# Performance work log

Hardware: AMD Instinct MI355X
Metric: run time of the kernel (lower is better)

## Reference

```python
import jax, jax.numpy as jnp
import numpy as np

N_QUBITS = 10
N_LAYERS = 2
BATCH = 8192
N_PARAMS = 5 * N_QUBITS * N_LAYERS  # 100
C64 = jnp.complex64

# ---- batched 2x2 gate matrices (theta: (B,)) ----

def _rx(theta):
    h = theta * 0.5
    c = jnp.cos(h).astype(C64)
    s = (-1j * jnp.sin(h).astype(C64))
    return jnp.stack([jnp.stack([c, s], -1), jnp.stack([s, c], -1)], -2)

def _ry(theta):
    h = theta * 0.5
    c = jnp.cos(h).astype(C64)
    s = jnp.sin(h).astype(C64)
    return jnp.stack([jnp.stack([c, -s], -1), jnp.stack([s, c], -1)], -2)

def _rz(theta):
    h = theta.astype(jnp.float32) * 0.5
    e0 = jnp.exp(-1j * h.astype(C64))
    e1 = jnp.exp(1j * h.astype(C64))
    z = jnp.zeros_like(e0)
    return jnp.stack([jnp.stack([e0, z], -1), jnp.stack([z, e1], -1)], -2)

# psi layout: (B, 2, 2, ..., 2); axis 1+w corresponds to wire w (PennyLane order: wire 0 = MSB)

def _apply_1q(psi, mat, w):
    psi = jnp.moveaxis(psi, 1 + w, -1)
    sh = psi.shape
    out = jnp.einsum('bij,bkj->bki', mat, psi.reshape(sh[0], -1, 2))
    return jnp.moveaxis(out.reshape(sh), -1, 1 + w)

def _apply_crx(psi, theta, ctrl, tgt):
    psi = jnp.moveaxis(psi, [1 + ctrl, 1 + tgt], [-2, -1])
    sh = psi.shape
    p = psi.reshape(sh[0], -1, 2, 2)  # axes: (batch, rest, ctrl, tgt)
    h = theta * 0.5
    c = jnp.cos(h)[:, None].astype(C64)
    s = (-1j * jnp.sin(h)[:, None].astype(C64))
    a0 = p[..., 1, 0]
    a1 = p[..., 1, 1]
    p1 = jnp.stack([c * a0 + s * a1, s * a0 + c * a1], -1)
    p = jnp.stack([p[..., 0, :], p1], -2)
    return jnp.moveaxis(p.reshape(sh), [-2, -1], [1 + ctrl, 1 + tgt])

def _init_state(angles):
    B = angles.shape[0]
    psi = jnp.zeros((B, 2 ** N_QUBITS), C64).at[:, 0].set(1.0)
    psi = psi.reshape((B,) + (2,) * N_QUBITS)
    for i in range(N_QUBITS):  # RY input embedding
        psi = _apply_1q(psi, _ry(angles[:, i]), i)
    return psi

def _delta_layer(psi, params, dt, off):
    for i in range(N_QUBITS):
        psi = _apply_1q(psi, _rx(params[:, off] * dt), i)
        psi = _apply_1q(psi, _ry(params[:, off + 1] * dt), i)
        psi = _apply_1q(psi, _rz(params[:, off + 2] * dt), i)
        off += 3
    for i in range(N_QUBITS):
        psi = _apply_crx(psi, params[:, off], i, (i + 1) % N_QUBITS); off += 1
    for i in range(N_QUBITS - 1, -1, -1):
        psi = _apply_crx(psi, params[:, off], i, (i - 1) % N_QUBITS); off += 1
    return psi, off

def _backward_layer(psi, params, dt, off):
    for i in range(N_QUBITS - 1, -1, -1):
        psi = _apply_1q(psi, _rx(params[:, off] * dt), i)
        psi = _apply_1q(psi, _ry(params[:, off + 1] * dt), i)
        psi = _apply_1q(psi, _rz(params[:, off + 2] * dt), i)
        off += 3
    for i in range(N_QUBITS - 1, -1, -1):
        psi = _apply_crx(psi, params[:, off], i, (i - 1) % N_QUBITS); off += 1
    for i in range(N_QUBITS):
        psi = _apply_crx(psi, params[:, off], i, (i + 1) % N_QUBITS); off += 1
    return psi, off

def _unified_layer(psi, params, off):
    for i in range(N_QUBITS):
        psi = _apply_1q(psi, _rx(params[:, off]), i)
        psi = _apply_1q(psi, _ry(params[:, off + 1]), i)
        psi = _apply_1q(psi, _rz(params[:, off + 2]), i)
        off += 3
    for i in range(N_QUBITS):
        psi = _apply_crx(psi, params[:, off], i, (i + 1) % N_QUBITS); off += 1
    for i in range(N_QUBITS - 1, -1, -1):
        psi = _apply_crx(psi, params[:, off], i, (i - 1) % N_QUBITS); off += 1
    return psi, off

def _forward_circuit(angles, params, dt):
    psi = _init_state(angles); off = 0
    for _ in range(N_LAYERS):
        psi, off = _delta_layer(psi, params, dt, off)
    return psi.reshape(psi.shape[0], -1)

def _backward_circuit(angles, params, dt):
    psi = _init_state(angles); off = 0
    for _ in range(N_LAYERS):
        psi, off = _backward_layer(psi, params, dt, off)
    return psi.reshape(psi.shape[0], -1)

def _diagonal_circuit(angles, params):
    psi = _init_state(angles); off = 0
    for _ in range(N_LAYERS):
        psi, off = _unified_layer(psi, params, off)
    return psi.reshape(psi.shape[0], -1)

def _measure(psi_flat):
    # Pauli X/Y/Z expectations per qubit -> (B, 3*n_qubits), ordered [X..., Y..., Z...]
    B = psi_flat.shape[0]
    t = psi_flat.reshape((B,) + (2,) * N_QUBITS)
    Xs, Ys, Zs = [], [], []
    for w in range(N_QUBITS):
        p = jnp.moveaxis(t, 1 + w, -1).reshape(B, -1, 2)
        cross = jnp.sum(jnp.conj(p[..., 0]) * p[..., 1], axis=1)
        Xs.append(2.0 * cross.real)
        Ys.append(2.0 * cross.imag)
        Zs.append(jnp.sum(jnp.abs(p[..., 0]) ** 2 - jnp.abs(p[..., 1]) ** 2, axis=1))
    return jnp.stack(Xs + Ys + Zs, axis=1)

def setup_inputs() -> dict:
    key = jax.random.key(0)
    k1, k2, k3, k4, k5 = jax.random.split(key, 5)
    init_val = np.float32(1.0 / np.sqrt(3.0))
    return {
        'input_angles': jax.random.normal(k1, (BATCH, N_QUBITS), jnp.float32),
        'forward_params': jax.random.normal(k2, (BATCH, N_PARAMS), jnp.float32),
        'backward_params': jax.random.normal(k3, (BATCH, N_PARAMS), jnp.float32),
        'diagonal_params': jax.random.normal(k4, (BATCH, N_PARAMS), jnp.float32),
        'dt_scale': jax.random.uniform(k5, (BATCH,), jnp.float32),
        'alpha_real': jnp.asarray(init_val), 'alpha_imag': jnp.asarray(0.0, jnp.float32),
        'beta_real': jnp.asarray(init_val), 'beta_imag': jnp.asarray(0.0, jnp.float32),
        'gamma_real': jnp.asarray(init_val), 'gamma_imag': jnp.asarray(0.0, jnp.float32),
    }

def reference(input_angles, forward_params, backward_params, diagonal_params, dt_scale,
              alpha_real, alpha_imag, beta_real, beta_imag, gamma_real, gamma_imag):
    psi1 = _forward_circuit(input_angles, forward_params, dt_scale)
    psi2 = _backward_circuit(input_angles, backward_params, dt_scale)
    psi3 = _diagonal_circuit(input_angles, diagonal_params)
    alpha = jax.lax.complex(alpha_real, alpha_imag).astype(C64)
    beta = jax.lax.complex(beta_real, beta_imag).astype(C64)
    gamma = jax.lax.complex(gamma_real, gamma_imag).astype(C64)
    norm = jnp.sqrt(jnp.abs(alpha) ** 2 + jnp.abs(beta) ** 2 + jnp.abs(gamma) ** 2 + 1e-9).astype(C64)
    psi = (alpha / norm) * psi1 + (beta / norm) * psi2 + (gamma / norm) * psi3
    vnorm = jnp.linalg.norm(psi, axis=-1, keepdims=True) + 1e-9
    psi = psi / vnorm.astype(C64)
    return _measure(psi).astype(jnp.float32)
```

## Files before the change

kernel.cpp:

```cpp
#include <hip/hip_runtime.h>

#define NQ    10
#define NPRM  100
#define NBATCH 8192

using F2 = float2;

template<int LM>
__device__ __forceinline__ float lshf(float v) {
  if constexpr (LM == 1) {
    int r = __builtin_amdgcn_update_dpp(0, __builtin_bit_cast(int, v), 0xB1, 0xF, 0xF, true);
    return __builtin_bit_cast(float, r);
  } else if constexpr (LM == 2) {
    int r = __builtin_amdgcn_update_dpp(0, __builtin_bit_cast(int, v), 0x4E, 0xF, 0xF, true);
    return __builtin_bit_cast(float, r);
  } else if constexpr (LM == 8) {
    int r = __builtin_amdgcn_update_dpp(0, __builtin_bit_cast(int, v), 0x128, 0xF, 0xF, true);
    return __builtin_bit_cast(float, r);
  } else {
    return __shfl_xor(v, LM, 64);
  }
}



template<int P>
__device__ __forceinline__ void g_rx(F2* st, unsigned lane, float c, float s) {
  if constexpr (P < 4) {
    constexpr int m = 1 << P;
#pragma unroll
    for (int r = 0; r < 16; ++r) if (!(r & m)) {
      const int r1 = r | m;
      F2 a0 = st[r], a1 = st[r1];
      st[r]  = F2{c*a0.x + s*a1.y, c*a0.y - s*a1.x};
      st[r1] = F2{s*a0.y + c*a1.x, c*a1.y - s*a0.x};
    }
  } else {
    constexpr int lm = 1 << (P - 4);
#pragma unroll
    for (int r = 0; r < 16; ++r) {
      float mx = st[r].x, my = st[r].y;
      float ox = lshf<lm>(mx), oy = lshf<lm>(my);
      st[r] = F2{c*mx + s*oy, c*my - s*ox};
    }
  }
}


template<int P>
__device__ __forceinline__ void g_u(F2* st, unsigned lane, F2 u00, F2 u01) {
  if constexpr (P < 4) {
    constexpr int m = 1 << P;
#pragma unroll
    for (int r = 0; r < 16; ++r) if (!(r & m)) {
      const int r1 = r | m;
      F2 a0 = st[r], a1 = st[r1];
      st[r]  = F2{u00.x*a0.x - u00.y*a0.y + u01.x*a1.x - u01.y*a1.y,
                  u00.x*a0.y + u00.y*a0.x + u01.x*a1.y + u01.y*a1.x};
      st[r1] = F2{-u01.x*a0.x - u01.y*a0.y + u00.x*a1.x + u00.y*a1.y,
                  -u01.x*a0.y + u01.y*a0.x + u00.x*a1.y - u00.y*a1.x};
    }
  } else {
    constexpr int lm = 1 << (P - 4);
    const bool hi = (lane & lm) != 0;
    const float vax = u00.x,               vay = hi ? -u00.y : u00.y;
    const float vbx = hi ? -u01.x : u01.x, vby = u01.y;
#pragma unroll
    for (int r = 0; r < 16; ++r) {
      float mx = st[r].x, my = st[r].y;
      float ox = lshf<lm>(mx), oy = lshf<lm>(my);
      st[r] = F2{vax*mx - vay*my + vbx*ox - vby*oy,
                 vax*my + vay*mx + vbx*oy + vby*ox};
    }
  }
}


template<int TB, int CB>
__device__ __forceinline__ void g_crx(F2* st, unsigned lane, float c, float s) {
  if constexpr (CB >= 4) {
    const bool act = (lane >> (CB - 4)) & 1u;
    const float ce = act ? c : 1.0f;
    const float se = act ? s : 0.0f;
    g_rx<TB>(st, lane, ce, se);
  } else {
    constexpr int cm = 1 << CB;
    if constexpr (TB < 4) {
#pragma unroll
      for (int r = 0; r < 16; ++r) if ((r & cm) && !(r & (1 << TB))) {
        const int r1 = r | (1 << TB);
        F2 a0 = st[r], a1 = st[r1];
        st[r]  = F2{c*a0.x + s*a1.y, c*a0.y - s*a1.x};
        st[r1] = F2{s*a0.y + c*a1.x, c*a1.y - s*a0.x};
      }
    } else {
      constexpr int lm = 1 << (TB - 4);
#pragma unroll
      for (int r = 0; r < 16; ++r) if (r & cm) {
        float mx = st[r].x, my = st[r].y;
        float ox = lshf<lm>(mx), oy = lshf<lm>(my);
        st[r] = F2{c*mx + s*oy, c*my - s*ox};
      }
    }
  }
}


__device__ __forceinline__ void g_u_w(F2* st, unsigned lane, int w, F2 u00, F2 u01) {
  switch (w) {
    case 0: g_u<9>(st,lane,u00,u01); break;
    case 1: g_u<8>(st,lane,u00,u01); break;
    case 2: g_u<7>(st,lane,u00,u01); break;
    case 3: g_u<6>(st,lane,u00,u01); break;
    case 4: g_u<5>(st,lane,u00,u01); break;
    case 5: g_u<4>(st,lane,u00,u01); break;
    case 6: g_u<3>(st,lane,u00,u01); break;
    case 7: g_u<2>(st,lane,u00,u01); break;
    case 8: g_u<1>(st,lane,u00,u01); break;
    case 9: g_u<0>(st,lane,u00,u01); break;
  }
}

#define CRX_CASE(CW,TW) case (CW)*10+(TW): g_crx<9-(TW), 9-(CW)>(st,lane,c,s); break;
__device__ __forceinline__ void crx_w(F2* st, unsigned lane, int cw, int tw, float c, float s) {
  switch (cw * 10 + tw) {
    CRX_CASE(0,1) CRX_CASE(1,2) CRX_CASE(2,3) CRX_CASE(3,4) CRX_CASE(4,5)
    CRX_CASE(5,6) CRX_CASE(6,7) CRX_CASE(7,8) CRX_CASE(8,9) CRX_CASE(9,0)
    CRX_CASE(1,0) CRX_CASE(2,1) CRX_CASE(3,2) CRX_CASE(4,3) CRX_CASE(5,4)
    CRX_CASE(6,5) CRX_CASE(7,6) CRX_CASE(8,7) CRX_CASE(9,8) CRX_CASE(0,9)
  }
}

__device__ __forceinline__ void make_u(float ax, float ay, float az, F2& u00, F2& u01) {
  float ca, sa, cb, sb, cg, sg;
  __sincosf(ax*0.5f, &sa, &ca);
  __sincosf(ay*0.5f, &sb, &cb);
  __sincosf(az*0.5f, &sg, &cg);
  const float m00x =  cb*ca, m00y =  sb*sa;
  const float m01x = -sb*ca, m01y = -cb*sa;
  u00 = F2{m00x*cg + m00y*sg, m00y*cg - m00x*sg};
  u01 = F2{m01x*cg + m01y*sg, m01y*cg - m01x*sg};
}


__device__ __forceinline__ void layer_fwd(F2* st, unsigned lane, const float* P, float dt, int& off) {
#pragma unroll
  for (int i = 0; i < NQ; ++i) {
    F2 u00, u01;
    make_u(P[off]*dt, P[off+1]*dt, P[off+2]*dt, u00, u01);
    g_u_w(st, lane, i, u00, u01);
    off += 3;
  }
#pragma unroll
  for (int i = 0; i < NQ; ++i) {
    float s, c; __sincosf(P[off]*0.5f, &s, &c);
    crx_w(st, lane, i, (i+1)%NQ, c, s); ++off;
  }
#pragma unroll
  for (int i = NQ-1; i >= 0; --i) {
    float s, c; __sincosf(P[off]*0.5f, &s, &c);
    crx_w(st, lane, i, (i+NQ-1)%NQ, c, s); ++off;
  }
}

__device__ __forceinline__ void layer_bwd(F2* st, unsigned lane, const float* P, float dt, int& off) {
#pragma unroll
  for (int i = NQ-1; i >= 0; --i) {
    F2 u00, u01;
    make_u(P[off]*dt, P[off+1]*dt, P[off+2]*dt, u00, u01);
    g_u_w(st, lane, i, u00, u01);
    off += 3;
  }
#pragma unroll
  for (int i = NQ-1; i >= 0; --i) {
    float s, c; __sincosf(P[off]*0.5f, &s, &c);
    crx_w(st, lane, i, (i+NQ-1)%NQ, c, s); ++off;
  }
#pragma unroll
  for (int i = 0; i < NQ; ++i) {
    float s, c; __sincosf(P[off]*0.5f, &s, &c);
    crx_w(st, lane, i, (i+1)%NQ, c, s); ++off;
  }
}

__device__ __forceinline__ void init_state(F2* st, unsigned lane, const float* ang) {
  float cw[NQ], sw[NQ];
#pragma unroll
  for (int w = 0; w < NQ; ++w) __sincosf(ang[w]*0.5f, &sw[w], &cw[w]);
  float L = 1.0f;
#pragma unroll
  for (int q = 0; q < 6; ++q)
    L *= ((lane >> q) & 1u) ? sw[5-q] : cw[5-q];
#pragma unroll
  for (int r = 0; r < 16; ++r) {
    float R = L;
#pragma unroll
    for (int p = 0; p < 4; ++p)
      R *= ((r >> p) & 1) ? sw[9-p] : cw[9-p];
    st[r] = F2{R, 0.0f};
  }
}


template<int P>
__device__ __forceinline__ void meas(const F2* st, unsigned lane, float& X, float& Y, float& Z) {
  float cr = 0.f, ci = 0.f, z = 0.f;
  if constexpr (P < 4) {
    constexpr int m = 1 << P;
#pragma unroll
    for (int r = 0; r < 16; ++r) if (!(r & m)) {
      const int r1 = r | m;
      F2 a0 = st[r], a1 = st[r1];
      cr += a0.x*a1.x + a0.y*a1.y;
      ci += a0.x*a1.y - a0.y*a1.x;
      z  += (a0.x*a0.x + a0.y*a0.y) - (a1.x*a1.x + a1.y*a1.y);
    }
    cr *= 2.f; ci *= 2.f;
  } else {
    constexpr int lm = 1 << (P - 4);
    const bool hi = (lane & lm) != 0;
#pragma unroll
    for (int r = 0; r < 16; ++r) {
      float mx = st[r].x, my = st[r].y;
      float ox = lshf<lm>(mx), oy = lshf<lm>(my);
      float a0x = hi ? ox : mx, a0y = hi ? oy : my;
      float a1x = hi ? mx : ox, a1y = hi ? my : oy;
      cr += a0x*a1x + a0y*a1y;
      ci += a0x*a1y - a0y*a1x;
      float p2 = mx*mx + my*my;
      z += hi ? -p2 : p2;
    }
  }
  X = cr; Y = ci; Z = z;
}

__device__ __forceinline__ float wred(float v) {
  v += lshf<1>(v);
  v += lshf<2>(v);
  v += lshf<4>(v);
  v += lshf<8>(v);
  v += lshf<16>(v);
  v += lshf<32>(v);
  return v;
}


__global__ void __launch_bounds__(256) qsim_kernel(
    const float* __restrict__ angles, const float* __restrict__ fwdP,
    const float* __restrict__ bwdP,   const float* __restrict__ diagP,
    const float* __restrict__ dts,
    const float* __restrict__ ar, const float* __restrict__ ai,
    const float* __restrict__ br, const float* __restrict__ bi,
    const float* __restrict__ gr, const float* __restrict__ gi,
    float* __restrict__ out)
{
  const int tid = blockIdx.x * blockDim.x + threadIdx.x;
  const int b = tid >> 6;
  if (b >= NBATCH) return;
  const unsigned lane = threadIdx.x & 63u;
  const int bu = __builtin_amdgcn_readfirstlane(b);

  const float* ang = angles + bu * NQ;
  const float dt = dts[bu];

  const float arv = ar[0], aiv = ai[0], brv = br[0], biv = bi[0], grv = gr[0], giv = gi[0];
  const float nrm = sqrtf(arv*arv + aiv*aiv + brv*brv + biv*biv + grv*grv + giv*giv + 1e-9f);
  const F2 cA{arv/nrm, aiv/nrm}, cB{brv/nrm, biv/nrm}, cG{grv/nrm, giv/nrm};

  F2 st[16], acc[16];

  init_state(st, lane, ang);
  { int off = 0; const float* P = fwdP + bu*NPRM;
#pragma unroll
    for (int l = 0; l < 2; ++l) layer_fwd(st, lane, P, dt, off); }
#pragma unroll
  for (int r = 0; r < 16; ++r)
    acc[r] = F2{cA.x*st[r].x - cA.y*st[r].y, cA.x*st[r].y + cA.y*st[r].x};

  init_state(st, lane, ang);
  { int off = 0; const float* P = bwdP + bu*NPRM;
#pragma unroll
    for (int l = 0; l < 2; ++l) layer_bwd(st, lane, P, dt, off); }
#pragma unroll
  for (int r = 0; r < 16; ++r) {
    acc[r].x += cB.x*st[r].x - cB.y*st[r].y;
    acc[r].y += cB.x*st[r].y + cB.y*st[r].x;
  }

  init_state(st, lane, ang);
  { int off = 0; const float* P = diagP + bu*NPRM;
#pragma unroll
    for (int l = 0; l < 2; ++l) layer_fwd(st, lane, P, 1.0f, off); }
#pragma unroll
  for (int r = 0; r < 16; ++r) {
    acc[r].x += cG.x*st[r].x - cG.y*st[r].y;
    acc[r].y += cG.x*st[r].y + cG.y*st[r].x;
  }

  float n2 = 0.f;
#pragma unroll
  for (int r = 0; r < 16; ++r) n2 += acc[r].x*acc[r].x + acc[r].y*acc[r].y;
  n2 = wred(n2);
  const float inv = 1.0f / (sqrtf(n2) + 1e-9f);
#pragma unroll
  for (int r = 0; r < 16; ++r) { acc[r].x *= inv; acc[r].y *= inv; }

  float* o = out + b * 30;
#pragma unroll
  for (int w = 0; w < NQ; ++w) {
    float X, Y, Z;
    switch (w) {
      case 0: meas<9>(acc, lane, X, Y, Z); break;
      case 1: meas<8>(acc, lane, X, Y, Z); break;
      case 2: meas<7>(acc, lane, X, Y, Z); break;
      case 3: meas<6>(acc, lane, X, Y, Z); break;
      case 4: meas<5>(acc, lane, X, Y, Z); break;
      case 5: meas<4>(acc, lane, X, Y, Z); break;
      case 6: meas<3>(acc, lane, X, Y, Z); break;
      case 7: meas<2>(acc, lane, X, Y, Z); break;
      case 8: meas<1>(acc, lane, X, Y, Z); break;
      default: meas<0>(acc, lane, X, Y, Z); break;
    }
    X = wred(X); Y = wred(Y); Z = wred(Z);
    if (lane == 0) { o[w] = X; o[10 + w] = Y; o[20 + w] = Z; }
  }
}

extern "C" void kernel_launch(void* const* d_in, const int* in_sizes, int n_in,
                              void* d_out, int out_size, void* d_ws, size_t ws_size,
                              hipStream_t stream) {
  const float* angles = (const float*)d_in[0];
  const float* fwdP   = (const float*)d_in[1];
  const float* bwdP   = (const float*)d_in[2];
  const float* diagP  = (const float*)d_in[3];
  const float* dts    = (const float*)d_in[4];
  const float* ar     = (const float*)d_in[5];
  const float* ai     = (const float*)d_in[6];
  const float* br     = (const float*)d_in[7];
  const float* bi     = (const float*)d_in[8];
  const float* gr     = (const float*)d_in[9];
  const float* gi     = (const float*)d_in[10];
  float* out = (float*)d_out;

  const int threads = 256;
  const int blocks  = NBATCH / (threads / 64);
  qsim_kernel<<<blocks, threads, 0, stream>>>(
      angles, fwdP, bwdP, diagP, dts, ar, ai, br, bi, gr, gi, out);
}
```

Before: 257.3 us.

## Simulate forward and diagonal circuits together in packed float2 SoA lanes

The forward and diagonal circuits share the same gate structure, so both are now simulated in one pass. Each amplitude is stored as separate real and imaginary float2 vectors, where the x component holds the forward circuit and the y component holds the diagonal one, so the compiler can emit packed FP32 math (v_pk_fma_f32). This removes one full serial circuit simulation and turns the per-element complex math into packed operations. In exchange it doubles the live state registers during that pass, which risks register pressure and lower occupancy, and it still shuffles each half of the vector separately.

```diff
diff --git a/kernel.cpp b/kernel.cpp
--- a/kernel.cpp
+++ b/kernel.cpp
@@ -4,7 +4,10 @@
 #define NPRM  100
 #define NBATCH 8192
 
-using F2 = float2;
+using F2 = __attribute__((ext_vector_type(2))) float;
+
+__device__ __forceinline__ F2 mk2(float a, float b) { F2 v; v.x = a; v.y = b; return v; }
+
 
 template<int LM>
 __device__ __forceinline__ float lshf(float v) {
@@ -21,6 +24,10 @@
     return __shfl_xor(v, LM, 64);
   }
 }
+template<int LM>
+__device__ __forceinline__ F2 lshf2(F2 v) {
+  return mk2(lshf<LM>(v.x), lshf<LM>(v.y));
+}
 
 
 
@@ -32,8 +39,8 @@
     for (int r = 0; r < 16; ++r) if (!(r & m)) {
       const int r1 = r | m;
       F2 a0 = st[r], a1 = st[r1];
-      st[r]  = F2{c*a0.x + s*a1.y, c*a0.y - s*a1.x};
-      st[r1] = F2{s*a0.y + c*a1.x, c*a1.y - s*a0.x};
+      st[r]  = mk2(c*a0.x + s*a1.y, c*a0.y - s*a1.x);
+      st[r1] = mk2(s*a0.y + c*a1.x, c*a1.y - s*a0.x);
     }
   } else {
     constexpr int lm = 1 << (P - 4);
@@ -41,11 +48,10 @@
     for (int r = 0; r < 16; ++r) {
       float mx = st[r].x, my = st[r].y;
       float ox = lshf<lm>(mx), oy = lshf<lm>(my);
-      st[r] = F2{c*mx + s*oy, c*my - s*ox};
-    }
-  }
-}
-
+      st[r] = mk2(c*mx + s*oy, c*my - s*ox);
+    }
+  }
+}
 
 template<int P>
 __device__ __forceinline__ void g_u(F2* st, unsigned lane, F2 u00, F2 u01) {
@@ -55,10 +61,10 @@
     for (int r = 0; r < 16; ++r) if (!(r & m)) {
       const int r1 = r | m;
       F2 a0 = st[r], a1 = st[r1];
-      st[r]  = F2{u00.x*a0.x - u00.y*a0.y + u01.x*a1.x - u01.y*a1.y,
-                  u00.x*a0.y + u00.y*a0.x + u01.x*a1.y + u01.y*a1.x};
-      st[r1] = F2{-u01.x*a0.x - u01.y*a0.y + u00.x*a1.x + u00.y*a1.y,
-                  -u01.x*a0.y + u01.y*a0.x + u00.x*a1.y - u00.y*a1.x};
+      st[r]  = mk2(u00.x*a0.x - u00.y*a0.y + u01.x*a1.x - u01.y*a1.y,
+                   u00.x*a0.y + u00.y*a0.x + u01.x*a1.y + u01.y*a1.x);
+      st[r1] = mk2(-u01.x*a0.x - u01.y*a0.y + u00.x*a1.x + u00.y*a1.y,
+                   -u01.x*a0.y + u01.y*a0.x + u00.x*a1.y - u00.y*a1.x);
     }
   } else {
     constexpr int lm = 1 << (P - 4);
@@ -69,12 +75,11 @@
     for (int r = 0; r < 16; ++r) {
       float mx = st[r].x, my = st[r].y;
       float ox = lshf<lm>(mx), oy = lshf<lm>(my);
-      st[r] = F2{vax*mx - vay*my + vbx*ox - vby*oy,
-                 vax*my + vay*mx + vbx*oy + vby*ox};
-    }
-  }
-}
-
+      st[r] = mk2(vax*mx - vay*my + vbx*ox - vby*oy,
+                  vax*my + vay*mx + vbx*oy + vby*ox);
+    }
+  }
+}
 
 template<int TB, int CB>
 __device__ __forceinline__ void g_crx(F2* st, unsigned lane, float c, float s) {
@@ -90,8 +95,8 @@
       for (int r = 0; r < 16; ++r) if ((r & cm) && !(r & (1 << TB))) {
         const int r1 = r | (1 << TB);
         F2 a0 = st[r], a1 = st[r1];
-        st[r]  = F2{c*a0.x + s*a1.y, c*a0.y - s*a1.x};
-        st[r1] = F2{s*a0.y + c*a1.x, c*a1.y - s*a0.x};
+        st[r]  = mk2(c*a0.x + s*a1.y, c*a0.y - s*a1.x);
+        st[r1] = mk2(s*a0.y + c*a1.x, c*a1.y - s*a0.x);
       }
     } else {
       constexpr int lm = 1 << (TB - 4);
@@ -99,12 +104,11 @@
       for (int r = 0; r < 16; ++r) if (r & cm) {
         float mx = st[r].x, my = st[r].y;
         float ox = lshf<lm>(mx), oy = lshf<lm>(my);
-        st[r] = F2{c*mx + s*oy, c*my - s*ox};
+        st[r] = mk2(c*mx + s*oy, c*my - s*ox);
       }
     }
   }
 }
-
 
 __device__ __forceinline__ void g_u_w(F2* st, unsigned lane, int w, F2 u00, F2 u01) {
   switch (w) {
@@ -138,29 +142,8 @@
   __sincosf(az*0.5f, &sg, &cg);
   const float m00x =  cb*ca, m00y =  sb*sa;
   const float m01x = -sb*ca, m01y = -cb*sa;
-  u00 = F2{m00x*cg + m00y*sg, m00y*cg - m00x*sg};
-  u01 = F2{m01x*cg + m01y*sg, m01y*cg - m01x*sg};
-}
-
-
-__device__ __forceinline__ void layer_fwd(F2* st, unsigned lane, const float* P, float dt, int& off) {
-#pragma unroll
-  for (int i = 0; i < NQ; ++i) {
-    F2 u00, u01;
-    make_u(P[off]*dt, P[off+1]*dt, P[off+2]*dt, u00, u01);
-    g_u_w(st, lane, i, u00, u01);
-    off += 3;
-  }
-#pragma unroll
-  for (int i = 0; i < NQ; ++i) {
-    float s, c; __sincosf(P[off]*0.5f, &s, &c);
-    crx_w(st, lane, i, (i+1)%NQ, c, s); ++off;
-  }
-#pragma unroll
-  for (int i = NQ-1; i >= 0; --i) {
-    float s, c; __sincosf(P[off]*0.5f, &s, &c);
-    crx_w(st, lane, i, (i+NQ-1)%NQ, c, s); ++off;
-  }
+  u00 = mk2(m00x*cg + m00y*sg, m00y*cg - m00x*sg);
+  u01 = mk2(m01x*cg + m01y*sg, m01y*cg - m01x*sg);
 }
 
 __device__ __forceinline__ void layer_bwd(F2* st, unsigned lane, const float* P, float dt, int& off) {
@@ -197,7 +180,168 @@
 #pragma unroll
     for (int p = 0; p < 4; ++p)
       R *= ((r >> p) & 1) ? sw[9-p] : cw[9-p];
-    st[r] = F2{R, 0.0f};
+    st[r] = mk2(R, 0.0f);
+  }
+}
+
+
+struct UU { F2 x00, y00, x01, y01; };
+
+template<int P>
+__device__ __forceinline__ void g_u2(F2* sR, F2* sI, unsigned lane, UU u) {
+  if constexpr (P < 4) {
+    constexpr int m = 1 << P;
+#pragma unroll
+    for (int r = 0; r < 16; ++r) if (!(r & m)) {
+      const int r1 = r | m;
+      F2 R0 = sR[r], I0 = sI[r], R1 = sR[r1], I1 = sI[r1];
+      sR[r]  = u.x00*R0 - u.y00*I0 + u.x01*R1 - u.y01*I1;
+      sI[r]  = u.x00*I0 + u.y00*R0 + u.x01*I1 + u.y01*R1;
+      sR[r1] = u.x00*R1 + u.y00*I1 - u.x01*R0 - u.y01*I0;
+      sI[r1] = u.x00*I1 - u.y00*R1 - u.x01*I0 + u.y01*R0;
+    }
+  } else {
+    constexpr int lm = 1 << (P - 4);
+    const bool hi = (lane & lm) != 0;
+    const F2 vay = mk2(hi ? -u.y00.x : u.y00.x, hi ? -u.y00.y : u.y00.y);
+    const F2 vbx = mk2(hi ? -u.x01.x : u.x01.x, hi ? -u.x01.y : u.x01.y);
+#pragma unroll
+    for (int r = 0; r < 16; ++r) {
+      F2 R = sR[r], I = sI[r];
+      F2 oR = lshf2<lm>(R), oI = lshf2<lm>(I);
+      sR[r] = u.x00*R - vay*I + vbx*oR - u.y01*oI;
+      sI[r] = u.x00*I + vay*R + vbx*oI + u.y01*oR;
+    }
+  }
+}
+
+template<int P>
+__device__ __forceinline__ void g_rx2(F2* sR, F2* sI, unsigned lane, F2 C, F2 S) {
+  if constexpr (P < 4) {
+    constexpr int m = 1 << P;
+#pragma unroll
+    for (int r = 0; r < 16; ++r) if (!(r & m)) {
+      const int r1 = r | m;
+      F2 R0 = sR[r], I0 = sI[r], R1 = sR[r1], I1 = sI[r1];
+      sR[r]  = C*R0 + S*I1;
+      sI[r]  = C*I0 - S*R1;
+      sR[r1] = C*R1 + S*I0;
+      sI[r1] = C*I1 - S*R0;
+    }
+  } else {
+    constexpr int lm = 1 << (P - 4);
+#pragma unroll
+    for (int r = 0; r < 16; ++r) {
+      F2 R = sR[r], I = sI[r];
+      F2 oR = lshf2<lm>(R), oI = lshf2<lm>(I);
+      sR[r] = C*R + S*oI;
+      sI[r] = C*I - S*oR;
+    }
+  }
+}
+
+template<int TB, int CB>
+__device__ __forceinline__ void g_crx2(F2* sR, F2* sI, unsigned lane, F2 C, F2 S) {
+  if constexpr (CB >= 4) {
+    const bool act = (lane >> (CB - 4)) & 1u;
+    const F2 Ce = mk2(act ? C.x : 1.0f, act ? C.y : 1.0f);
+    const F2 Se = mk2(act ? S.x : 0.0f, act ? S.y : 0.0f);
+    g_rx2<TB>(sR, sI, lane, Ce, Se);
+  } else {
+    constexpr int cm = 1 << CB;
+    if constexpr (TB < 4) {
+#pragma unroll
+      for (int r = 0; r < 16; ++r) if ((r & cm) && !(r & (1 << TB))) {
+        const int r1 = r | (1 << TB);
+        F2 R0 = sR[r], I0 = sI[r], R1 = sR[r1], I1 = sI[r1];
+        sR[r]  = C*R0 + S*I1;
+        sI[r]  = C*I0 - S*R1;
+        sR[r1] = C*R1 + S*I0;
+        sI[r1] = C*I1 - S*R0;
+      }
+    } else {
+      constexpr int lm = 1 << (TB - 4);
+#pragma unroll
+      for (int r = 0; r < 16; ++r) if (r & cm) {
+        F2 R = sR[r], I = sI[r];
+        F2 oR = lshf2<lm>(R), oI = lshf2<lm>(I);
+        sR[r] = C*R + S*oI;
+        sI[r] = C*I - S*oR;
+      }
+    }
+  }
+}
+
+__device__ __forceinline__ void g_u2_w(F2* sR, F2* sI, unsigned lane, int w, UU u) {
+  switch (w) {
+    case 0: g_u2<9>(sR,sI,lane,u); break;
+    case 1: g_u2<8>(sR,sI,lane,u); break;
+    case 2: g_u2<7>(sR,sI,lane,u); break;
+    case 3: g_u2<6>(sR,sI,lane,u); break;
+    case 4: g_u2<5>(sR,sI,lane,u); break;
+    case 5: g_u2<4>(sR,sI,lane,u); break;
+    case 6: g_u2<3>(sR,sI,lane,u); break;
+    case 7: g_u2<2>(sR,sI,lane,u); break;
+    case 8: g_u2<1>(sR,sI,lane,u); break;
+    case 9: g_u2<0>(sR,sI,lane,u); break;
+  }
+}
+
+#define CRX2_CASE(CW,TW) case (CW)*10+(TW): g_crx2<9-(TW), 9-(CW)>(sR,sI,lane,C,S); break;
+__device__ __forceinline__ void crx2_w(F2* sR, F2* sI, unsigned lane, int cw, int tw, F2 C, F2 S) {
+  switch (cw * 10 + tw) {
+    CRX2_CASE(0,1) CRX2_CASE(1,2) CRX2_CASE(2,3) CRX2_CASE(3,4) CRX2_CASE(4,5)
+    CRX2_CASE(5,6) CRX2_CASE(6,7) CRX2_CASE(7,8) CRX2_CASE(8,9) CRX2_CASE(9,0)
+    CRX2_CASE(1,0) CRX2_CASE(2,1) CRX2_CASE(3,2) CRX2_CASE(4,3) CRX2_CASE(5,4)
+    CRX2_CASE(6,5) CRX2_CASE(7,6) CRX2_CASE(8,7) CRX2_CASE(9,8) CRX2_CASE(0,9)
+  }
+}
+
+__device__ __forceinline__ void layer_fwd2(F2* sR, F2* sI, unsigned lane,
+                                           const float* Pf, const float* Pd, float dt, int& off) {
+#pragma unroll
+  for (int i = 0; i < NQ; ++i) {
+    F2 u00F, u01F, u00D, u01D;
+    make_u(Pf[off]*dt, Pf[off+1]*dt, Pf[off+2]*dt, u00F, u01F);
+    make_u(Pd[off],    Pd[off+1],    Pd[off+2],    u00D, u01D);
+    UU u;
+    u.x00 = mk2(u00F.x, u00D.x); u.y00 = mk2(u00F.y, u00D.y);
+    u.x01 = mk2(u01F.x, u01D.x); u.y01 = mk2(u01F.y, u01D.y);
+    g_u2_w(sR, sI, lane, i, u);
+    off += 3;
+  }
+#pragma unroll
+  for (int i = 0; i < NQ; ++i) {
+    float sF, cF, sD, cD;
+    __sincosf(Pf[off]*0.5f, &sF, &cF);
+    __sincosf(Pd[off]*0.5f, &sD, &cD);
+    crx2_w(sR, sI, lane, i, (i+1)%NQ, mk2(cF,cD), mk2(sF,sD)); ++off;
+  }
+#pragma unroll
+  for (int i = NQ-1; i >= 0; --i) {
+    float sF, cF, sD, cD;
+    __sincosf(Pf[off]*0.5f, &sF, &cF);
+    __sincosf(Pd[off]*0.5f, &sD, &cD);
+    crx2_w(sR, sI, lane, i, (i+NQ-1)%NQ, mk2(cF,cD), mk2(sF,sD)); ++off;
+  }
+}
+
+__device__ __forceinline__ void init_state2(F2* sR, F2* sI, unsigned lane, const float* ang) {
+  float cw[NQ], sw[NQ];
+#pragma unroll
+  for (int w = 0; w < NQ; ++w) __sincosf(ang[w]*0.5f, &sw[w], &cw[w]);
+  float L = 1.0f;
+#pragma unroll
+  for (int q = 0; q < 6; ++q)
+    L *= ((lane >> q) & 1u) ? sw[5-q] : cw[5-q];
+#pragma unroll
+  for (int r = 0; r < 16; ++r) {
+    float R = L;
+#pragma unroll
+    for (int p = 0; p < 4; ++p)
+      R *= ((r >> p) & 1) ? sw[9-p] : cw[9-p];
+    sR[r] = mk2(R, R);
+    sI[r] = mk2(0.0f, 0.0f);
   }
 }
 
@@ -265,61 +409,57 @@
 
   const float arv = ar[0], aiv = ai[0], brv = br[0], biv = bi[0], grv = gr[0], giv = gi[0];
   const float nrm = sqrtf(arv*arv + aiv*aiv + brv*brv + biv*biv + grv*grv + giv*giv + 1e-9f);
-  const F2 cA{arv/nrm, aiv/nrm}, cB{brv/nrm, biv/nrm}, cG{grv/nrm, giv/nrm};
-
-  F2 st[16], acc[16];
-
-  init_state(st, lane, ang);
-  { int off = 0; const float* P = fwdP + bu*NPRM;
-#pragma unroll
-    for (int l = 0; l < 2; ++l) layer_fwd(st, lane, P, dt, off); }
-#pragma unroll
-  for (int r = 0; r < 16; ++r)
-    acc[r] = F2{cA.x*st[r].x - cA.y*st[r].y, cA.x*st[r].y + cA.y*st[r].x};
-
+  const F2 cA = mk2(arv/nrm, aiv/nrm), cB = mk2(brv/nrm, biv/nrm), cG = mk2(grv/nrm, giv/nrm);
+
+  F2 sR[16], sI[16];
+  init_state2(sR, sI, lane, ang);
+  { int off = 0;
+    const float* Pf = fwdP  + bu*NPRM;
+    const float* Pd = diagP + bu*NPRM;
+#pragma unroll
+    for (int l = 0; l < 2; ++l) layer_fwd2(sR, sI, lane, Pf, Pd, dt, off); }
+
+  F2 stc[16];
+#pragma unroll
+  for (int r = 0; r < 16; ++r) {
+    stc[r] = mk2(cA.x*sR[r].x - cA.y*sI[r].x + cG.x*sR[r].y - cG.y*sI[r].y,
+                 cA.x*sI[r].x + cA.y*sR[r].x + cG.x*sI[r].y + cG.y*sR[r].y);
+  }
+
+  F2 st[16];
   init_state(st, lane, ang);
   { int off = 0; const float* P = bwdP + bu*NPRM;
 #pragma unroll
     for (int l = 0; l < 2; ++l) layer_bwd(st, lane, P, dt, off); }
 #pragma unroll
   for (int r = 0; r < 16; ++r) {
-    acc[r].x += cB.x*st[r].x - cB.y*st[r].y;
-    acc[r].y += cB.x*st[r].y + cB.y*st[r].x;
-  }
-
-  init_state(st, lane, ang);
-  { int off = 0; const float* P = diagP + bu*NPRM;
-#pragma unroll
-    for (int l = 0; l < 2; ++l) layer_fwd(st, lane, P, 1.0f, off); }
-#pragma unroll
-  for (int r = 0; r < 16; ++r) {
-    acc[r].x += cG.x*st[r].x - cG.y*st[r].y;
-    acc[r].y += cG.x*st[r].y + cG.y*st[r].x;
+    stc[r] = mk2(stc[r].x + cB.x*st[r].x - cB.y*st[r].y,
+                 stc[r].y + cB.x*st[r].y + cB.y*st[r].x);
   }
 
   float n2 = 0.f;
 #pragma unroll
-  for (int r = 0; r < 16; ++r) n2 += acc[r].x*acc[r].x + acc[r].y*acc[r].y;
+  for (int r = 0; r < 16; ++r) n2 += stc[r].x*stc[r].x + stc[r].y*stc[r].y;
   n2 = wred(n2);
   const float inv = 1.0f / (sqrtf(n2) + 1e-9f);
 #pragma unroll
-  for (int r = 0; r < 16; ++r) { acc[r].x *= inv; acc[r].y *= inv; }
+  for (int r = 0; r < 16; ++r) { stc[r] = mk2(stc[r].x*inv, stc[r].y*inv); }
 
   float* o = out + b * 30;
 #pragma unroll
   for (int w = 0; w < NQ; ++w) {
     float X, Y, Z;
     switch (w) {
-      case 0: meas<9>(acc, lane, X, Y, Z); break;
-      case 1: meas<8>(acc, lane, X, Y, Z); break;
-      case 2: meas<7>(acc, lane, X, Y, Z); break;
-      case 3: meas<6>(acc, lane, X, Y, Z); break;
-      case 4: meas<5>(acc, lane, X, Y, Z); break;
-      case 5: meas<4>(acc, lane, X, Y, Z); break;
-      case 6: meas<3>(acc, lane, X, Y, Z); break;
-      case 7: meas<2>(acc, lane, X, Y, Z); break;
-      case 8: meas<1>(acc, lane, X, Y, Z); break;
-      default: meas<0>(acc, lane, X, Y, Z); break;
+      case 0: meas<9>(stc, lane, X, Y, Z); break;
+      case 1: meas<8>(stc, lane, X, Y, Z); break;
+      case 2: meas<7>(stc, lane, X, Y, Z); break;
+      case 3: meas<6>(stc, lane, X, Y, Z); break;
+      case 4: meas<5>(stc, lane, X, Y, Z); break;
+      case 5: meas<4>(stc, lane, X, Y, Z); break;
+      case 6: meas<3>(stc, lane, X, Y, Z); break;
+      case 7: meas<2>(stc, lane, X, Y, Z); break;
+      case 8: meas<1>(stc, lane, X, Y, Z); break;
+      default: meas<0>(stc, lane, X, Y, Z); break;
     }
     X = wred(X); Y = wred(Y); Z = wred(Z);
     if (lane == 0) { o[w] = X; o[10 + w] = Y; o[20 + w] = Z; }
```

Measured after the change: 289.2 us. +12.4%, slower.
